# Kernel tuning notes

Hardware: AMD Instinct MI355X
Metric: run time of the kernel (lower is better)

Reference implementation:

```python
import jax, jax.numpy as jnp
import numpy as np

B, L, D, H = 4, 4096, 1024, 16
Dh = D // H
DECAY_INIT, DECAY_RANGE = 5.0, 1.0
LN_EPS = 1e-5


def setup_inputs() -> dict:
    key = jax.random.key(0)
    ks = jax.random.split(key, 5)
    s = 1.0 / np.sqrt(D)
    x = jax.random.normal(ks[0], (B, L, D), dtype=jnp.float32)
    Wq = jax.random.normal(ks[1], (D, D), dtype=jnp.float32) * s
    Wv = jax.random.normal(ks[2], (D, D), dtype=jnp.float32) * s
    Wo = jax.random.normal(ks[3], (D, D), dtype=jnp.float32) * s
    Wg = jax.random.normal(ks[4], (D, D), dtype=jnp.float32) * s
    # per-head decay logits, matching __init__: 5.0 + 1.0 * h / H
    beta = DECAY_INIT + DECAY_RANGE * (jnp.arange(H, dtype=jnp.float32) / H)
    ln_gamma = jnp.ones((D,), dtype=jnp.float32)
    ln_beta = jnp.zeros((D,), dtype=jnp.float32)
    return {"x": x, "Wq": Wq, "Wv": Wv, "Wo": Wo, "Wg": Wg,
            "beta": beta, "ln_gamma": ln_gamma, "ln_beta": ln_beta}


def _retention_scan(v, lam):
    # v: (B,L,H,Dh), lam: (H,); s_t = lam * s_{t-1} + v_t  (s_{-1} = 0)
    a = jnp.broadcast_to(lam[None, None, :, None], v.shape)

    def combine(c1, c2):
        a1, b1 = c1
        a2, b2 = c2
        return a1 * a2, a2 * b1 + b2

    _, s = jax.lax.associative_scan(combine, (a, v), axis=1)
    return s


def _layernorm(x, gamma, beta):
    mu = jnp.mean(x, axis=-1, keepdims=True)
    var = jnp.mean(jnp.square(x - mu), axis=-1, keepdims=True)
    return (x - mu) * jax.lax.rsqrt(var + LN_EPS) * gamma + beta


def reference(x, Wq, Wv, Wo, Wg, beta, ln_gamma, ln_beta):
    b, l, d = x.shape
    # decay lambda per head: (1 - 2^-beta) clamped to (tiny, 1 - 1e-9)
    tiny = jnp.finfo(jnp.float32).tiny
    lam = jnp.clip(1.0 - jnp.exp2(-beta), tiny, 1.0 - 1e-9)
    q = (x @ Wq.T).reshape(b, l, H, Dh)
    v = (x @ Wv.T).reshape(b, l, H, Dh)
    state = _retention_scan(v, lam)             # (B,L,H,Dh)
    ret = (q * state).reshape(b, l, d)          # per-timestep retention readout
    y = _layernorm(ret, ln_gamma, ln_beta)
    g = jax.nn.silu(x @ Wg.T)                   # swish gate
    out = (y * g) @ Wo.T
    return out
```

## Files before the change

### kernel.cpp

```cpp
#include <hip/hip_runtime.h>
#include <hip/hip_bf16.h>
#include <cfloat>

#define BB 4
#define LL 4096
#define DD 1024
#define HH 16
#define DHH 64
#define MM (BB * LL)
#define LN_EPS 1e-5f
#define LDQVG 3072
#define SCC 16
#define NCHUNK (LL / SCC)

typedef __hip_bfloat16 bf16;
typedef __attribute__((ext_vector_type(8))) short short8;
typedef __attribute__((ext_vector_type(16))) float float16_t;

struct bf16x4 { bf16 a, b, c, d; };
struct alignas(16) bf8 { bf16 e[8]; };

__device__ __forceinline__ float b2f(bf16 u) {
    union { unsigned int i; float f; } c;
    c.i = ((unsigned int)__bfloat16_as_ushort(u)) << 16;
    return c.f;
}

__device__ __forceinline__ float lam_of(const float* beta, int head) {
    float lam = 1.0f - exp2f(-beta[head]);
    return fminf(fmaxf(lam, 1.1754944e-38f), 1.0f - 1e-9f);
}

__global__ __launch_bounds__(256) void cvt_f32_bf16(const float* __restrict__ in,
                                                    bf16* __restrict__ out, int n) {
    int i = (blockIdx.x * 256 + threadIdx.x) * 4;
    if (i >= n) return;
    float4 f = *(const float4*)(in + i);
    bf16x4 o;
    o.a = __float2bfloat16(f.x);
    o.b = __float2bfloat16(f.y);
    o.c = __float2bfloat16(f.z);
    o.d = __float2bfloat16(f.w);
    *(bf16x4*)(out + i) = o;
}

__global__ __launch_bounds__(256) void cvt4_weights(const float* __restrict__ w0,
                                                    const float* __restrict__ w1,
                                                    const float* __restrict__ w2,
                                                    const float* __restrict__ w3,
                                                    bf16* __restrict__ o) {
    int which = blockIdx.x >> 10;
    int i = ((blockIdx.x & 1023) * 256 + threadIdx.x) * 4;
    const float* w = (which == 0) ? w0 : (which == 1) ? w1 : (which == 2) ? w2 : w3;
    float4 f = *(const float4*)(w + i);
    bf16x4 r;
    r.a = __float2bfloat16(f.x);
    r.b = __float2bfloat16(f.y);
    r.c = __float2bfloat16(f.z);
    r.d = __float2bfloat16(f.w);
    *(bf16x4*)(o + (size_t)which * 1048576 + i) = r;
}

__device__ __forceinline__ void async16(const bf16* g, bf16* l) {
    __builtin_amdgcn_global_load_lds(
        (const __attribute__((address_space(1))) void*)g,
        (__attribute__((address_space(3))) void*)l,
        16, 0, 0);
}

template <typename OutT, int KK>
__global__ __launch_bounds__(256) void gemm_bt(const bf16* __restrict__ A,
                                               const bf16* __restrict__ Bm,
                                               OutT* __restrict__ C,
                                               int M, int N, int ldc) {
    __shared__ bf16 sA[128 * 64];
    __shared__ bf16 sB[128 * 64];

    const int t    = threadIdx.x;
    const int lane = t & 63;
    const int wave = t >> 6;
    const int wm   = (wave >> 1) * 64;
    const int wn   = (wave & 1) * 64;

    const int bm = blockIdx.x;
    const int bn = blockIdx.y;

    const bf16* gA[4];
    const bf16* gB[4];
    bf16* lA[4];
    bf16* lB[4];
#pragma unroll
    for (int j = 0; j < 4; ++j) {
        int c = t + j * 256;
        int r = c >> 3;
        int g = ((c & 7) - (r & 7)) & 7;
        gA[j] = A  + (size_t)(bm * 128 + r) * KK + g * 8;
        gB[j] = Bm + (size_t)(bn * 128 + r) * KK + g * 8;
        lA[j] = sA + c * 8;
        lB[j] = sB + c * 8;
    }

    const int kh = lane >> 5;
    const bf16* rdA[2][4];
    const bf16* rdB[2][4];
#pragma unroll
    for (int mi = 0; mi < 2; ++mi) {
        int r = wm + (lane & 31) + mi * 32;
#pragma unroll
        for (int tk = 0; tk < 4; ++tk) {
            int kc = tk * 2 + kh;
            rdA[mi][tk] = sA + (r * 8 + ((kc + r) & 7)) * 8;
        }
    }
#pragma unroll
    for (int ni = 0; ni < 2; ++ni) {
        int r = wn + (lane & 31) + ni * 32;
#pragma unroll
        for (int tk = 0; tk < 4; ++tk) {
            int kc = tk * 2 + kh;
            rdB[ni][tk] = sB + (r * 8 + ((kc + r) & 7)) * 8;
        }
    }

    float16_t acc[2][2] = {};

#pragma unroll 1
    for (int it = 0; it < KK / 64; ++it) {
#pragma unroll
        for (int j = 0; j < 4; ++j) async16(gA[j], lA[j]);
#pragma unroll
        for (int j = 0; j < 4; ++j) async16(gB[j], lB[j]);
#pragma unroll
        for (int j = 0; j < 4; ++j) { gA[j] += 64; gB[j] += 64; }
        __syncthreads();

#pragma unroll
        for (int tk = 0; tk < 4; ++tk) {
            short8 a0 = *(const short8*)rdA[0][tk];
            short8 a1 = *(const short8*)rdA[1][tk];
            short8 b0 = *(const short8*)rdB[0][tk];
            short8 b1 = *(const short8*)rdB[1][tk];
            acc[0][0] = __builtin_amdgcn_mfma_f32_32x32x16_bf16(a0, b0, acc[0][0], 0, 0, 0);
            acc[0][1] = __builtin_amdgcn_mfma_f32_32x32x16_bf16(a0, b1, acc[0][1], 0, 0, 0);
            acc[1][0] = __builtin_amdgcn_mfma_f32_32x32x16_bf16(a1, b0, acc[1][0], 0, 0, 0);
            acc[1][1] = __builtin_amdgcn_mfma_f32_32x32x16_bf16(a1, b1, acc[1][1], 0, 0, 0);
        }
        __syncthreads();
    }

    const int col0 = bn * 128 + wn + (lane & 31);
    const int row0 = bm * 128 + wm + 4 * (lane >> 5);
#pragma unroll
    for (int mi = 0; mi < 2; ++mi) {
#pragma unroll
        for (int ni = 0; ni < 2; ++ni) {
#pragma unroll
            for (int reg = 0; reg < 16; ++reg) {
                int row = row0 + mi * 32 + (reg & 3) + 8 * (reg >> 2);
                C[(size_t)row * ldc + col0 + ni * 32] = (OutT)acc[mi][ni][reg];
            }
        }
    }
}

__global__ __launch_bounds__(64) void scan_chunksum(const bf16* __restrict__ qvg,
                                                    const float* __restrict__ beta,
                                                    float* __restrict__ S) {
    const int c    = blockIdx.x;
    const int half = blockIdx.y;
    const int b    = blockIdx.z;
    const int tid  = threadIdx.x;
    const int dh0  = half * 512 + tid * 8;
    const float lam = lam_of(beta, dh0 >> 6);

    const bf16* vp = qvg + 1024 + ((size_t)(b * LL + c * SCC)) * LDQVG + dh0;

    float s[8] = {};
#pragma unroll
    for (int t = 0; t < SCC; ++t) {
        bf8 vv = *(const bf8*)(vp + (size_t)t * LDQVG);
#pragma unroll
        for (int j = 0; j < 8; ++j)
            s[j] = fmaf(s[j], lam, b2f(vv.e[j]));
    }

    float* sp = S + ((size_t)(b * NCHUNK + c)) * DD + dh0;
    float4 lo = {s[0], s[1], s[2], s[3]};
    float4 hi = {s[4], s[5], s[6], s[7]};
    *(float4*)(sp)     = lo;
    *(float4*)(sp + 4) = hi;
}

__global__ __launch_bounds__(64) void scan_carry(const float* __restrict__ S,
                                                 float* __restrict__ T,
                                                 const float* __restrict__ beta) {
    const int gid = blockIdx.x * 64 + threadIdx.x;
    const int b = gid >> 10;
    const int f = gid & 1023;
    const float lam  = lam_of(beta, f >> 6);
    const float lamC = powf(lam, (float)SCC);

    const size_t base = (size_t)b * NCHUNK * DD + f;
    float t = 0.0f;
    for (int c = 0; c < NCHUNK; ++c) {
        float s = S[base + (size_t)c * DD];
        T[base + (size_t)c * DD] = t;
        t = fmaf(t, lamC, s);
    }
}

__global__ __launch_bounds__(64) void scan_apply(bf16* __restrict__ qvg,
                                                 const float* __restrict__ beta,
                                                 const float* __restrict__ T) {
    const int c    = blockIdx.x;
    const int half = blockIdx.y;
    const int b    = blockIdx.z;
    const int tid  = threadIdx.x;
    const int dh0  = half * 512 + tid * 8;
    const float lam = lam_of(beta, dh0 >> 6);

    const float* tp = T + ((size_t)(b * NCHUNK + c)) * DD + dh0;
    float4 lo = *(const float4*)(tp);
    float4 hi = *(const float4*)(tp + 4);
    float s[8] = {lo.x, lo.y, lo.z, lo.w, hi.x, hi.y, hi.z, hi.w};

    bf16* qp = qvg + ((size_t)(b * LL + c * SCC)) * LDQVG + dh0;

#pragma unroll
    for (int t = 0; t < SCC; ++t) {
        const size_t off = (size_t)t * LDQVG;
        bf8 vv = *(const bf8*)(qp + 1024 + off);
        bf8 qq = *(const bf8*)(qp + off);
        bf8 o;
#pragma unroll
        for (int j = 0; j < 8; ++j) {
            s[j] = fmaf(s[j], lam, b2f(vv.e[j]));
            o.e[j] = __float2bfloat16(b2f(qq.e[j]) * s[j]);
        }
        *(bf8*)(qp + off) = o;
    }
}

__global__ __launch_bounds__(256) void ln_gate(const bf16* __restrict__ qvg,
                                               const float* __restrict__ gamma,
                                               const float* __restrict__ betaln,
                                               bf16* __restrict__ z) {
    const int row  = blockIdx.x;
    const int tid  = threadIdx.x;
    const int lane = tid & 63;
    const int wave = tid >> 6;
    const size_t rbase = (size_t)row * LDQVG + tid * 4;

    bf16x4 rv = *(const bf16x4*)(qvg + rbase);
    float x0 = b2f(rv.a), x1 = b2f(rv.b), x2 = b2f(rv.c), x3 = b2f(rv.d);

    float s  = x0 + x1 + x2 + x3;
    float s2 = x0 * x0 + x1 * x1 + x2 * x2 + x3 * x3;
#pragma unroll
    for (int off = 32; off >= 1; off >>= 1) {
        s  += __shfl_xor(s, off, 64);
        s2 += __shfl_xor(s2, off, 64);
    }
    __shared__ float red[8];
    if (lane == 0) { red[wave] = s; red[wave + 4] = s2; }
    __syncthreads();
    s  = red[0] + red[1] + red[2] + red[3];
    s2 = red[4] + red[5] + red[6] + red[7];

    const float mu   = s * (1.0f / DD);
    const float var  = s2 * (1.0f / DD) - mu * mu;
    const float rstd = rsqrtf(var + LN_EPS);

    bf16x4 gv = *(const bf16x4*)(qvg + rbase + 2048);
    float4 gm = *(const float4*)(gamma + tid * 4);
    float4 bt = *(const float4*)(betaln + tid * 4);

    float xs[4]  = {x0, x1, x2, x3};
    float gs[4]  = {b2f(gv.a), b2f(gv.b), b2f(gv.c), b2f(gv.d)};
    float gmm[4] = {gm.x, gm.y, gm.z, gm.w};
    float btt[4] = {bt.x, bt.y, bt.z, bt.w};

    bf16x4 o;
    bf16* op = &o.a;
#pragma unroll
    for (int j = 0; j < 4; ++j) {
        float y  = (xs[j] - mu) * rstd * gmm[j] + btt[j];
        float g  = gs[j];
        float sg = g / (1.0f + expf(-g));
        op[j] = __float2bfloat16(y * sg);
    }
    *(bf16x4*)(z + (size_t)row * DD + tid * 4) = o;
}

extern "C" void kernel_launch(void* const* d_in, const int* in_sizes, int n_in,
                              void* d_out, int out_size, void* d_ws, size_t ws_size,
                              hipStream_t stream) {
    const float* x     = (const float*)d_in[0];
    const float* Wq    = (const float*)d_in[1];
    const float* Wv    = (const float*)d_in[2];
    const float* Wo    = (const float*)d_in[3];
    const float* Wg    = (const float*)d_in[4];
    const float* beta  = (const float*)d_in[5];
    const float* ln_g  = (const float*)d_in[6];
    const float* ln_b  = (const float*)d_in[7];
    float* out = (float*)d_out;

    char* ws = (char*)d_ws;
    bf16*  xb   = (bf16*)ws;
    float* Sbuf = (float*)ws;
    float* Tbuf = (float*)(ws + (size_t)4 * 1024 * 1024);
    bf16*  wqb  = (bf16*)(ws + (size_t)32 * 1024 * 1024);
    bf16*  wob  = wqb + 3 * 1048576;
    bf16*  qvg  = (bf16*)(ws + (size_t)40 * 1024 * 1024);
    bf16*  zb   = xb;

    cvt_f32_bf16<<<dim3((MM * DD) / 1024), dim3(256), 0, stream>>>(x, xb, MM * DD);
    cvt4_weights<<<dim3(4096), dim3(256), 0, stream>>>(Wq, Wv, Wg, Wo, wqb);

    gemm_bt<bf16, DD><<<dim3(MM / 128, LDQVG / 128), dim3(256), 0, stream>>>(
        xb, wqb, qvg, MM, LDQVG, LDQVG);

    scan_chunksum<<<dim3(NCHUNK, 2, BB), dim3(64), 0, stream>>>(qvg, beta, Sbuf);
    scan_carry<<<dim3(64), dim3(64), 0, stream>>>(Sbuf, Tbuf, beta);
    scan_apply<<<dim3(NCHUNK, 2, BB), dim3(64), 0, stream>>>(qvg, beta, Tbuf);

    ln_gate<<<dim3(MM), dim3(256), 0, stream>>>(qvg, ln_g, ln_b, zb);

    gemm_bt<float, DD><<<dim3(MM / 128, DD / 128), dim3(256), 0, stream>>>(
        zb, wob, out, MM, DD, DD);
}
```

Baseline: 349.8 us.

## Fuse scan apply with layernorm gate, merge conversions, prefetch carry scan

Merges the scan-apply and layernorm/gate kernels so retention outputs for a chunk of 16 rows stay in LDS. This avoids writing them back into the qvg buffer and rereading them. It also merges the input and weight bf16 conversions into one launch and software-prefetches chunk sums in the serial carry scan. The fused kernel runs only 1024 blocks of 128 threads with 32KB of LDS each, so occupancy and parallelism are lower than in the separate kernels. Tbuf is moved onto the weight region, which is only safe because the QVG GEMM has already consumed those weights; Wo lives at a later offset and is untouched.

```diff
diff --git a/kernel.cpp b/kernel.cpp
--- a/kernel.cpp
+++ b/kernel.cpp
@@ -31,34 +31,34 @@
     return fminf(fmaxf(lam, 1.1754944e-38f), 1.0f - 1e-9f);
 }
 
-__global__ __launch_bounds__(256) void cvt_f32_bf16(const float* __restrict__ in,
-                                                    bf16* __restrict__ out, int n) {
-    int i = (blockIdx.x * 256 + threadIdx.x) * 4;
-    if (i >= n) return;
-    float4 f = *(const float4*)(in + i);
+__global__ __launch_bounds__(256) void cvt_all(const float* __restrict__ x,
+                                               const float* __restrict__ wq,
+                                               const float* __restrict__ wv,
+                                               const float* __restrict__ wg,
+                                               const float* __restrict__ wo,
+                                               bf16* __restrict__ xb,
+                                               bf16* __restrict__ wb) {
+    const int blk = blockIdx.x;
+    const float* src;
+    bf16* dst;
+    size_t off;
+    if (blk < 16384) {
+        src = x; dst = xb; off = (size_t)blk * 1024;
+    } else {
+        int wblk  = blk - 16384;
+        int which = wblk >> 10;
+        src = (which == 0) ? wq : (which == 1) ? wv : (which == 2) ? wg : wo;
+        dst = wb + (size_t)which * 1048576;
+        off = (size_t)(wblk & 1023) * 1024;
+    }
+    size_t i = off + threadIdx.x * 4;
+    float4 f = *(const float4*)(src + i);
     bf16x4 o;
     o.a = __float2bfloat16(f.x);
     o.b = __float2bfloat16(f.y);
     o.c = __float2bfloat16(f.z);
     o.d = __float2bfloat16(f.w);
-    *(bf16x4*)(out + i) = o;
-}
-
-__global__ __launch_bounds__(256) void cvt4_weights(const float* __restrict__ w0,
-                                                    const float* __restrict__ w1,
-                                                    const float* __restrict__ w2,
-                                                    const float* __restrict__ w3,
-                                                    bf16* __restrict__ o) {
-    int which = blockIdx.x >> 10;
-    int i = ((blockIdx.x & 1023) * 256 + threadIdx.x) * 4;
-    const float* w = (which == 0) ? w0 : (which == 1) ? w1 : (which == 2) ? w2 : w3;
-    float4 f = *(const float4*)(w + i);
-    bf16x4 r;
-    r.a = __float2bfloat16(f.x);
-    r.b = __float2bfloat16(f.y);
-    r.c = __float2bfloat16(f.z);
-    r.d = __float2bfloat16(f.w);
-    *(bf16x4*)(o + (size_t)which * 1048576 + i) = r;
+    *(bf16x4*)(dst + i) = o;
 }
 
 __device__ __forceinline__ void async16(const bf16* g, bf16* l) {
@@ -201,31 +201,49 @@
     const float lamC = powf(lam, (float)SCC);
 
     const size_t base = (size_t)b * NCHUNK * DD + f;
+
+    float v[8];
+#pragma unroll
+    for (int j = 0; j < 8; ++j) v[j] = S[base + (size_t)j * DD];
+
     float t = 0.0f;
-    for (int c = 0; c < NCHUNK; ++c) {
-        float s = S[base + (size_t)c * DD];
-        T[base + (size_t)c * DD] = t;
-        t = fmaf(t, lamC, s);
-    }
-}
-
-__global__ __launch_bounds__(64) void scan_apply(bf16* __restrict__ qvg,
-                                                 const float* __restrict__ beta,
-                                                 const float* __restrict__ T) {
-    const int c    = blockIdx.x;
-    const int half = blockIdx.y;
-    const int b    = blockIdx.z;
-    const int tid  = threadIdx.x;
-    const int dh0  = half * 512 + tid * 8;
-    const float lam = lam_of(beta, dh0 >> 6);
-
-    const float* tp = T + ((size_t)(b * NCHUNK + c)) * DD + dh0;
+    for (int c0 = 0; c0 < NCHUNK; c0 += 8) {
+        float cur[8];
+#pragma unroll
+        for (int j = 0; j < 8; ++j) cur[j] = v[j];
+        if (c0 + 8 < NCHUNK) {
+#pragma unroll
+            for (int j = 0; j < 8; ++j)
+                v[j] = S[base + (size_t)(c0 + 8 + j) * DD];
+        }
+#pragma unroll
+        for (int j = 0; j < 8; ++j) {
+            T[base + (size_t)(c0 + j) * DD] = t;
+            t = fmaf(t, lamC, cur[j]);
+        }
+    }
+}
+
+__global__ __launch_bounds__(128) void scan_apply_ln(const bf16* __restrict__ qvg,
+                                                     const float* __restrict__ beta,
+                                                     const float* __restrict__ T,
+                                                     const float* __restrict__ gamma,
+                                                     const float* __restrict__ betaln,
+                                                     bf16* __restrict__ z) {
+    __shared__ bf16 lds_ret[SCC][DD];
+
+    const int c   = blockIdx.x;
+    const int b   = blockIdx.y;
+    const int tid = threadIdx.x;
+    const int f0  = tid * 8;
+    const float lam = lam_of(beta, f0 >> 6);
+
+    const float* tp = T + ((size_t)(b * NCHUNK + c)) * DD + f0;
     float4 lo = *(const float4*)(tp);
     float4 hi = *(const float4*)(tp + 4);
     float s[8] = {lo.x, lo.y, lo.z, lo.w, hi.x, hi.y, hi.z, hi.w};
 
-    bf16* qp = qvg + ((size_t)(b * LL + c * SCC)) * LDQVG + dh0;
-
+    const bf16* qp = qvg + ((size_t)(b * LL + c * SCC)) * LDQVG + f0;
 #pragma unroll
     for (int t = 0; t < SCC; ++t) {
         const size_t off = (size_t)t * LDQVG;
@@ -237,59 +255,63 @@
             s[j] = fmaf(s[j], lam, b2f(vv.e[j]));
             o.e[j] = __float2bfloat16(b2f(qq.e[j]) * s[j]);
         }
-        *(bf8*)(qp + off) = o;
-    }
-}
-
-__global__ __launch_bounds__(256) void ln_gate(const bf16* __restrict__ qvg,
-                                               const float* __restrict__ gamma,
-                                               const float* __restrict__ betaln,
-                                               bf16* __restrict__ z) {
-    const int row  = blockIdx.x;
-    const int tid  = threadIdx.x;
+        *(bf8*)(&lds_ret[t][f0]) = o;
+    }
+    __syncthreads();
+
     const int lane = tid & 63;
-    const int wave = tid >> 6;
-    const size_t rbase = (size_t)row * LDQVG + tid * 4;
-
-    bf16x4 rv = *(const bf16x4*)(qvg + rbase);
-    float x0 = b2f(rv.a), x1 = b2f(rv.b), x2 = b2f(rv.c), x3 = b2f(rv.d);
-
-    float s  = x0 + x1 + x2 + x3;
-    float s2 = x0 * x0 + x1 * x1 + x2 * x2 + x3 * x3;
-#pragma unroll
-    for (int off = 32; off >= 1; off >>= 1) {
-        s  += __shfl_xor(s, off, 64);
-        s2 += __shfl_xor(s2, off, 64);
-    }
-    __shared__ float red[8];
-    if (lane == 0) { red[wave] = s; red[wave + 4] = s2; }
-    __syncthreads();
-    s  = red[0] + red[1] + red[2] + red[3];
-    s2 = red[4] + red[5] + red[6] + red[7];
-
-    const float mu   = s * (1.0f / DD);
-    const float var  = s2 * (1.0f / DD) - mu * mu;
-    const float rstd = rsqrtf(var + LN_EPS);
-
-    bf16x4 gv = *(const bf16x4*)(qvg + rbase + 2048);
-    float4 gm = *(const float4*)(gamma + tid * 4);
-    float4 bt = *(const float4*)(betaln + tid * 4);
-
-    float xs[4]  = {x0, x1, x2, x3};
-    float gs[4]  = {b2f(gv.a), b2f(gv.b), b2f(gv.c), b2f(gv.d)};
-    float gmm[4] = {gm.x, gm.y, gm.z, gm.w};
-    float btt[4] = {bt.x, bt.y, bt.z, bt.w};
-
-    bf16x4 o;
-    bf16* op = &o.a;
-#pragma unroll
-    for (int j = 0; j < 4; ++j) {
-        float y  = (xs[j] - mu) * rstd * gmm[j] + btt[j];
-        float g  = gs[j];
-        float sg = g / (1.0f + expf(-g));
-        op[j] = __float2bfloat16(y * sg);
-    }
-    *(bf16x4*)(z + (size_t)row * DD + tid * 4) = o;
+    const int wv   = tid >> 6;
+
+    float gmA[8], btA[8], gmB[8], btB[8];
+#pragma unroll
+    for (int j = 0; j < 8; j += 4) {
+        *(float4*)(gmA + j) = *(const float4*)(gamma  + lane * 8 + j);
+        *(float4*)(btA + j) = *(const float4*)(betaln + lane * 8 + j);
+        *(float4*)(gmB + j) = *(const float4*)(gamma  + 512 + lane * 8 + j);
+        *(float4*)(btB + j) = *(const float4*)(betaln + 512 + lane * 8 + j);
+    }
+
+    for (int t = wv; t < SCC; t += 2) {
+        bf8 rA = *(const bf8*)(&lds_ret[t][lane * 8]);
+        bf8 rB = *(const bf8*)(&lds_ret[t][512 + lane * 8]);
+
+        float xa[8], xb2[8];
+        float sum = 0.f, sq = 0.f;
+#pragma unroll
+        for (int j = 0; j < 8; ++j) {
+            xa[j]  = b2f(rA.e[j]);
+            xb2[j] = b2f(rB.e[j]);
+            sum += xa[j] + xb2[j];
+            sq  += xa[j] * xa[j] + xb2[j] * xb2[j];
+        }
+#pragma unroll
+        for (int off = 32; off >= 1; off >>= 1) {
+            sum += __shfl_xor(sum, off, 64);
+            sq  += __shfl_xor(sq,  off, 64);
+        }
+        const float mu   = sum * (1.0f / DD);
+        const float var  = sq * (1.0f / DD) - mu * mu;
+        const float rstd = rsqrtf(var + LN_EPS);
+
+        const size_t row = (size_t)(b * LL + c * SCC + t);
+        const bf16* gp = qvg + row * LDQVG + 2048 + lane * 8;
+        bf8 gA = *(const bf8*)(gp);
+        bf8 gB = *(const bf8*)(gp + 512);
+
+        bf8 oA, oB;
+#pragma unroll
+        for (int j = 0; j < 8; ++j) {
+            float ya = (xa[j]  - mu) * rstd * gmA[j] + btA[j];
+            float yb = (xb2[j] - mu) * rstd * gmB[j] + btB[j];
+            float ga = b2f(gA.e[j]);
+            float gb = b2f(gB.e[j]);
+            oA.e[j] = __float2bfloat16(ya * (ga / (1.0f + expf(-ga))));
+            oB.e[j] = __float2bfloat16(yb * (gb / (1.0f + expf(-gb))));
+        }
+        bf16* zp = z + row * DD + lane * 8;
+        *(bf8*)(zp)       = oA;
+        *(bf8*)(zp + 512) = oB;
+    }
 }
 
 extern "C" void kernel_launch(void* const* d_in, const int* in_sizes, int n_in,
@@ -308,23 +330,21 @@
     char* ws = (char*)d_ws;
     bf16*  xb   = (bf16*)ws;
     float* Sbuf = (float*)ws;
-    float* Tbuf = (float*)(ws + (size_t)4 * 1024 * 1024);
     bf16*  wqb  = (bf16*)(ws + (size_t)32 * 1024 * 1024);
+    float* Tbuf = (float*)(ws + (size_t)32 * 1024 * 1024);
     bf16*  wob  = wqb + 3 * 1048576;
     bf16*  qvg  = (bf16*)(ws + (size_t)40 * 1024 * 1024);
     bf16*  zb   = xb;
 
-    cvt_f32_bf16<<<dim3((MM * DD) / 1024), dim3(256), 0, stream>>>(x, xb, MM * DD);
-    cvt4_weights<<<dim3(4096), dim3(256), 0, stream>>>(Wq, Wv, Wg, Wo, wqb);
+    cvt_all<<<dim3(16384 + 4096), dim3(256), 0, stream>>>(x, Wq, Wv, Wg, Wo, xb, wqb);
 
     gemm_bt<bf16, DD><<<dim3(MM / 128, LDQVG / 128), dim3(256), 0, stream>>>(
         xb, wqb, qvg, MM, LDQVG, LDQVG);
 
     scan_chunksum<<<dim3(NCHUNK, 2, BB), dim3(64), 0, stream>>>(qvg, beta, Sbuf);
     scan_carry<<<dim3(64), dim3(64), 0, stream>>>(Sbuf, Tbuf, beta);
-    scan_apply<<<dim3(NCHUNK, 2, BB), dim3(64), 0, stream>>>(qvg, beta, Tbuf);
-
-    ln_gate<<<dim3(MM), dim3(256), 0, stream>>>(qvg, ln_g, ln_b, zb);
+    scan_apply_ln<<<dim3(NCHUNK, BB), dim3(128), 0, stream>>>(
+        qvg, beta, Tbuf, ln_g, ln_b, zb);
 
     gemm_bt<float, DD><<<dim3(MM / 128, DD / 128), dim3(256), 0, stream>>>(
         zb, wob, out, MM, DD, DD);
```

New measurement: 348.7 us. Within noise of the previous version (-0.3%).
